# Optimization experiments

Measured on AMD Instinct MI355X. Metric: run time of the kernel, lower is better.

Reference implementation:

```python
import jax, jax.numpy as jnp
import numpy as np

B, L, D = 32, 2048, 512


def setup_inputs() -> dict:
    key = jax.random.key(0)
    kx, ka, kb, kc = jax.random.split(key, 4)
    scale = 0.5 / np.sqrt(D)  # keep recurrence spectral radius < 1 over L steps
    x = jax.random.normal(kx, (B, L, D), dtype=jnp.float32)
    deltaA = jax.random.normal(ka, (D, D), dtype=jnp.float32) * scale
    deltaB = jax.random.normal(kb, (D, D), dtype=jnp.float32) * scale
    C = jax.random.normal(kc, (D, D), dtype=jnp.float32) * scale
    return {"x": x, "deltaA": deltaA, "deltaB": deltaB, "C": C}


def reference(x, deltaA, deltaB, C):
    b, l, d = x.shape
    # Pre-project inputs with one big GEMM: u_t = x_t @ deltaB  -> [b, l, d]
    u = jnp.einsum('bld,de->ble', x, deltaB)

    def step(h, u_t):
        # h_t = h_{t-1} @ deltaA + x_t @ deltaB
        h = h @ deltaA + u_t
        return h, h

    h0 = jnp.zeros((b, d), dtype=x.dtype)
    # scan over time axis: u as [l, b, d]
    _, hs = jax.lax.scan(step, h0, jnp.swapaxes(u, 0, 1))  # hs: [l, b, d]
    # y_t = h_t @ C, one big GEMM after the scan
    y = jnp.einsum('lbd,de->lbe', hs, C)
    return jnp.swapaxes(y, 0, 1)  # [b, l, d]
```

## Files before the change

### kernel.cpp

```cpp
#include <hip/hip_runtime.h>


using bf16 = __bf16;
typedef __bf16 bf16x8 __attribute__((ext_vector_type(8)));
typedef float  f32x4  __attribute__((ext_vector_type(4)));
typedef unsigned int u32;

constexpr int Dm   = 512;
constexpr int Lseq = 2048;
constexpr int KC   = 8;
constexpr int CH   = 256;

__device__ __forceinline__ bf16x8 ld8(const bf16* p) {
  return *reinterpret_cast<const bf16x8*>(p);
}
__device__ __forceinline__ bf16x8 ld8f(const float* p) {
  f32x4 lo = *reinterpret_cast<const f32x4*>(p);
  f32x4 hi = *reinterpret_cast<const f32x4*>(p + 4);
  bf16x8 r;
#pragma unroll
  for (int i = 0; i < 4; ++i) { r[i] = (bf16)lo[i]; r[i + 4] = (bf16)hi[i]; }
  return r;
}
__device__ __forceinline__ f32x4 mfma16(bf16x8 a, bf16x8 b, f32x4 c) {
  return __builtin_amdgcn_mfma_f32_16x16x32_bf16(a, b, c, 0, 0, 0);
}
__device__ __forceinline__ void gld16(const bf16* g, bf16* l) {
  __builtin_amdgcn_global_load_lds(
      (const __attribute__((address_space(1))) u32*)g,
      (__attribute__((address_space(3))) u32*)l, 16, 0, 0);
}

template<int WM, int WN>
__device__ __forceinline__ void mma_step(const bf16* As, const bf16* Bs,
                                         int arow, int brow, int sw, int quad,
                                         f32x4 (&acc)[WM][WN]) {
#pragma unroll
  for (int ks = 0; ks < 2; ++ks) {
    const int sg = ((ks * 4 + quad) ^ sw) * 8;
    bf16x8 a[WM], b[WN];
#pragma unroll
    for (int m = 0; m < WM; ++m) a[m] = ld8(As + arow + m * 1024 + sg);
#pragma unroll
    for (int n = 0; n < WN; ++n) b[n] = ld8(Bs + brow + n * 1024 + sg);
#pragma unroll
    for (int m = 0; m < WM; ++m)
#pragma unroll
      for (int n = 0; n < WN; ++n) acc[m][n] = mfma16(a[m], b[n], acc[m][n]);
  }
}

__global__ __launch_bounds__(256) void kt_pack(
    const float* __restrict__ a, const float* __restrict__ b, const float* __restrict__ c,
    bf16* __restrict__ at, bf16* __restrict__ bt, bf16* __restrict__ ct,
    bf16* __restrict__ abf, bf16* __restrict__ zrow) {
  if (blockIdx.y == 0 && blockIdx.x == 0 && threadIdx.x < 256)
    reinterpret_cast<int*>(zrow)[threadIdx.x] = 0;
  int flat = blockIdx.x * 256 + threadIdx.x;
  int n = flat & (Dm - 1);
  int k = flat >> 9;
  const float* s = (blockIdx.y == 0) ? a : (blockIdx.y == 1) ? b : c;
  bf16* d        = (blockIdx.y == 0) ? at : (blockIdx.y == 1) ? bt : ct;
  float v = s[(long)k * Dm + n];
  d[(long)n * Dm + k] = (bf16)v;
  if (blockIdx.y == 0) abf[(long)k * Dm + n] = (bf16)v;
}

__global__ __launch_bounds__(256) void kt_cvt(
    const float* __restrict__ x, bf16* __restrict__ xb) {
  const long total = (long)32 * Lseq * Dm;
  for (long i = ((long)blockIdx.x * 256 + threadIdx.x) * 8; i < total;
       i += (long)2048 * 256 * 8)
    *reinterpret_cast<bf16x8*>(xb + i) = ld8f(x + i);
}

__global__ __launch_bounds__(256) void kt_u(
    const bf16* __restrict__ xb, const bf16* __restrict__ Bt, bf16* __restrict__ u) {
  __shared__ __align__(16) char LDSraw[36864];
  bf16* As = (bf16*)LDSraw;
  bf16* Bs = As + 128 * 64;
  const int tid = threadIdx.x, wave = tid >> 6, lane = tid & 63;
  const int quad = lane >> 4, l16 = lane & 15;
  const int seg = tid & 7, rr0 = tid >> 3;
  const int m0 = blockIdx.x * 128, n0 = blockIdx.y * 128;
  bf16* aL = As + wave * 512;
  bf16* bL = Bs + wave * 512;
  const int wrB = (wave >> 1) * 64, wcB = (wave & 1) * 64;
  const int arow = (wrB + l16) * 64, brow = (wcB + l16) * 64, sw = l16 & 7;
  f32x4 acc[4][4] = {};
  const bf16* aSrc[4]; const bf16* bSrc[4];
#pragma unroll
  for (int it = 0; it < 4; ++it) {
    int r = it * 32 + rr0;
    int sg = seg ^ (r & 7);
    aSrc[it] = xb + (long)(m0 + r) * Dm + sg * 8;
    bSrc[it] = Bt + (long)(n0 + r) * Dm + sg * 8;
  }
  for (int k0 = 0; k0 < Dm; k0 += 64) {
#pragma unroll
    for (int it = 0; it < 4; ++it) {
      gld16(aSrc[it] + k0, aL + it * 2048);
      gld16(bSrc[it] + k0, bL + it * 2048);
    }
    __syncthreads();
    mma_step<4, 4>(As, Bs, arow, brow, sw, quad, acc);
    __syncthreads();
  }
  bf16* smB = (bf16*)LDSraw;
#pragma unroll
  for (int m = 0; m < 4; ++m)
#pragma unroll
    for (int n = 0; n < 4; ++n)
#pragma unroll
      for (int r = 0; r < 4; ++r)
        smB[(wrB + m * 16 + quad * 4 + r) * 136 + wcB + n * 16 + l16] =
            (bf16)acc[m][n][r];
  __syncthreads();
#pragma unroll
  for (int it = 0; it < 8; ++it) {
    int chunk = it * 256 + tid;
    int row = chunk >> 4, c16 = chunk & 15;
    bf16x8 v = ld8(&smB[row * 136 + c16 * 8]);
    *reinterpret_cast<bf16x8*>(u + (long)(m0 + row) * Dm + n0 + c16 * 8) = v;
  }
}

__global__ __launch_bounds__(512) void kt_square(
    const bf16* __restrict__ P, const bf16* __restrict__ Pt,
    bf16* __restrict__ S, bf16* __restrict__ St) {
  const int tid = threadIdx.x;
  const int wave = tid >> 6, lane = tid & 63;
  const int quad = lane >> 4, l16 = lane & 15;
  const long rowbase = (long)blockIdx.x * 32;
  const int nbase = wave * 64;
  f32x4 acc[2][4] = {};
  for (int kk = 0; kk < Dm; kk += 32) {
    const int kf = kk + quad * 8;
    bf16x8 a0 = ld8(P + (rowbase + l16) * Dm + kf);
    bf16x8 a1 = ld8(P + (rowbase + 16 + l16) * Dm + kf);
#pragma unroll
    for (int nt = 0; nt < 4; ++nt) {
      bf16x8 bw = ld8(Pt + (long)(nbase + nt * 16 + l16) * Dm + kf);
      acc[0][nt] = mfma16(a0, bw, acc[0][nt]);
      acc[1][nt] = mfma16(a1, bw, acc[1][nt]);
    }
  }
#pragma unroll
  for (int mt = 0; mt < 2; ++mt)
#pragma unroll
    for (int nt = 0; nt < 4; ++nt)
#pragma unroll
      for (int r = 0; r < 4; ++r) {
        long m = rowbase + mt * 16 + quad * 4 + r;
        int n = nbase + nt * 16 + l16;
        float v = acc[mt][nt][r];
        S[m * Dm + n] = (bf16)v;
        St[(long)n * Dm + m] = (bf16)v;
      }
}

__global__ __launch_bounds__(512) void kt_taps(
    const bf16* __restrict__ q1, const bf16* __restrict__ q2,
    const bf16* __restrict__ q3, const bf16* __restrict__ q4,
    const bf16* __restrict__ q5, const bf16* __restrict__ q6,
    const bf16* __restrict__ q7, const bf16* __restrict__ q8,
    const bf16* __restrict__ Ct, bf16* __restrict__ Tt) {
  const int j = blockIdx.y;
  const bf16* Aop = (j == 0) ? q1 : (j == 1) ? q2 : (j == 2) ? q3 : (j == 3) ? q4
                  : (j == 4) ? q5 : (j == 5) ? q6 : (j == 6) ? q7 : q8;
  bf16* St = Tt + (long)j * Dm * Dm;
  const int tid = threadIdx.x;
  const int wave = tid >> 6, lane = tid & 63;
  const int quad = lane >> 4, l16 = lane & 15;
  const long rowbase = (long)blockIdx.x * 32;
  const int nbase = wave * 64;
  f32x4 acc[2][4] = {};
  for (int kk = 0; kk < Dm; kk += 32) {
    const int kf = kk + quad * 8;
    bf16x8 a0 = ld8(Aop + (rowbase + l16) * Dm + kf);
    bf16x8 a1 = ld8(Aop + (rowbase + 16 + l16) * Dm + kf);
#pragma unroll
    for (int nt = 0; nt < 4; ++nt) {
      bf16x8 bw = ld8(Ct + (long)(nbase + nt * 16 + l16) * Dm + kf);
      acc[0][nt] = mfma16(a0, bw, acc[0][nt]);
      acc[1][nt] = mfma16(a1, bw, acc[1][nt]);
    }
  }
#pragma unroll
  for (int mt = 0; mt < 2; ++mt)
#pragma unroll
    for (int nt = 0; nt < 4; ++nt)
#pragma unroll
      for (int r = 0; r < 4; ++r) {
        long m = rowbase + mt * 16 + quad * 4 + r;
        int n = nbase + nt * 16 + l16;
        St[(long)n * Dm + m] = (bf16)acc[mt][nt][r];
      }
}

__global__ __launch_bounds__(256) void kt_step(
    const bf16* __restrict__ u, const bf16* __restrict__ prevB,
    const bf16* __restrict__ At, bf16* __restrict__ hall, int j) {
  __shared__ __align__(16) bf16 As[64 * 64];
  __shared__ __align__(16) bf16 Bs[64 * 64];
  const int tid = threadIdx.x, wave = tid >> 6, lane = tid & 63;
  const int quad = lane >> 4, l16 = lane & 15;
  const int seg = tid & 7, rr0 = tid >> 3;
  const int m0 = blockIdx.x * 64, n0 = blockIdx.y * 64;
  const int b = m0 >> 8, c0 = m0 & 255;
  const bf16* aSrc[2]; const bf16* bSrc[2];
#pragma unroll
  for (int it = 0; it < 2; ++it) {
    int r = it * 32 + rr0;
    int sg = seg ^ (r & 7);
    aSrc[it] = prevB + ((long)b * Lseq + (long)(c0 + r) * KC + (j - 1)) * Dm + sg * 8;
    bSrc[it] = At + (long)(n0 + r) * Dm + sg * 8;
  }
  bf16* aL = As + wave * 512;
  bf16* bL = Bs + wave * 512;
  const int wrB = (wave >> 1) * 32, wcB = (wave & 1) * 32;
  const int arow = (wrB + l16) * 64, brow = (wcB + l16) * 64, sw = l16 & 7;
  f32x4 acc[2][2] = {};
  for (int k0 = 0; k0 < Dm; k0 += 64) {
#pragma unroll
    for (int it = 0; it < 2; ++it) {
      gld16(aSrc[it] + k0, aL + it * 2048);
      gld16(bSrc[it] + k0, bL + it * 2048);
    }
    __syncthreads();
    mma_step<2, 2>(As, Bs, arow, brow, sw, quad, acc);
    __syncthreads();
  }
#pragma unroll
  for (int m = 0; m < 2; ++m)
#pragma unroll
    for (int n = 0; n < 2; ++n)
#pragma unroll
      for (int r = 0; r < 4; ++r) {
        int row = wrB + m * 16 + quad * 4 + r;
        int col = n0 + wcB + n * 16 + l16;
        long off = ((long)b * Lseq + (long)(c0 + row) * KC + j) * Dm + col;
        hall[off] = (bf16)(acc[m][n][r] + (float)u[off]);
      }
}

__global__ __launch_bounds__(256) void kt_ks(
    const bf16* __restrict__ HinB, long sb, long sc, long off0,
    bf16* __restrict__ Hout, const bf16* __restrict__ Qt,
    const bf16* __restrict__ Q, const bf16* __restrict__ zrow,
    bf16* __restrict__ Snext, bf16* __restrict__ SnextT,
    int shift, int doSq) {
  __shared__ __align__(16) bf16 As[64 * 64];
  __shared__ __align__(16) bf16 Bs[64 * 64];
  const int tid = threadIdx.x, wave = tid >> 6, lane = tid & 63;
  const int quad = lane >> 4, l16 = lane & 15;
  const int seg = tid & 7, rr0 = tid >> 3;
  bf16* aL = As + wave * 512;
  bf16* bL = Bs + wave * 512;
  const int wrB = (wave >> 1) * 32, wcB = (wave & 1) * 32;
  const int arow = (wrB + l16) * 64, brow = (wcB + l16) * 64, sw = l16 & 7;
  f32x4 acc[2][2] = {};
  if (blockIdx.y < 8) {
    const int m0 = blockIdx.x * 64, n0 = blockIdx.y * 64;
    const int b = m0 >> 8, c0 = m0 & 255;
    const bf16* aSrc[2]; const bf16* bSrc[2];
#pragma unroll
    for (int it = 0; it < 2; ++it) {
      int r = it * 32 + rr0;
      int sg = seg ^ (r & 7);
      int c = c0 + r - shift;
      aSrc[it] = (c >= 0) ? HinB + ((long)b * sb + (long)c * sc + off0) * Dm + sg * 8
                          : zrow + sg * 8;
      bSrc[it] = Qt + (long)(n0 + r) * Dm + sg * 8;
    }
    for (int k0 = 0; k0 < Dm; k0 += 64) {
#pragma unroll
      for (int it = 0; it < 2; ++it) {
        gld16(aSrc[it] + k0, aL + it * 2048);
        gld16(bSrc[it] + k0, bL + it * 2048);
      }
      __syncthreads();
      mma_step<2, 2>(As, Bs, arow, brow, sw, quad, acc);
      __syncthreads();
    }
#pragma unroll
    for (int m = 0; m < 2; ++m)
#pragma unroll
      for (int n = 0; n < 2; ++n)
#pragma unroll
        for (int r = 0; r < 4; ++r) {
          int row = wrB + m * 16 + quad * 4 + r;
          int col = n0 + wcB + n * 16 + l16;
          int c = c0 + row;
          float v = acc[m][n][r] +
                    (float)HinB[((long)b * sb + (long)c * sc + off0) * Dm + col];
          Hout[((long)(b * 256 + c)) * Dm + col] = (bf16)v;
        }
  } else {
    if (blockIdx.x >= 64 || !doSq) return;
    const int m0 = (blockIdx.x >> 3) * 64, n0 = (blockIdx.x & 7) * 64;
    const bf16* aSrc[2]; const bf16* bSrc[2];
#pragma unroll
    for (int it = 0; it < 2; ++it) {
      int r = it * 32 + rr0;
      int sg = seg ^ (r & 7);
      aSrc[it] = Q + (long)(m0 + r) * Dm + sg * 8;
      bSrc[it] = Qt + (long)(n0 + r) * Dm + sg * 8;
    }
    for (int k0 = 0; k0 < Dm; k0 += 64) {
#pragma unroll
      for (int it = 0; it < 2; ++it) {
        gld16(aSrc[it] + k0, aL + it * 2048);
        gld16(bSrc[it] + k0, bL + it * 2048);
      }
      __syncthreads();
      mma_step<2, 2>(As, Bs, arow, brow, sw, quad, acc);
      __syncthreads();
    }
#pragma unroll
    for (int m = 0; m < 2; ++m)
#pragma unroll
      for (int n = 0; n < 2; ++n)
#pragma unroll
        for (int r = 0; r < 4; ++r) {
          int mg = m0 + wrB + m * 16 + quad * 4 + r;
          int ng = n0 + wcB + n * 16 + l16;
          float v = acc[m][n][r];
          Snext[(long)mg * Dm + ng] = (bf16)v;
          SnextT[(long)ng * Dm + mg] = (bf16)v;
        }
  }
}

__global__ __launch_bounds__(256) void kt_out(
    const bf16* __restrict__ hall, const bf16* __restrict__ u,
    const bf16* __restrict__ P, const bf16* __restrict__ Ct,
    const bf16* __restrict__ Tt, const bf16* __restrict__ zrow,
    float* __restrict__ y) {
  __shared__ __align__(16) char LDSraw[32768];
  bf16* As = (bf16*)LDSraw;
  bf16* Bs = As + 128 * 64;
  const int tid = threadIdx.x, wave = tid >> 6, lane = tid & 63;
  const int quad = lane >> 4, l16 = lane & 15;
  const int seg = tid & 7, rr0 = tid >> 3;
  const int m0 = blockIdx.x * 128, n0 = blockIdx.y * 128;
  const int j = blockIdx.z;
  const int b = m0 >> 8, c0 = m0 & 255;
  bf16* aL = As + wave * 512;
  bf16* bL = Bs + wave * 512;
  const int wrB = (wave >> 1) * 64, wcB = (wave & 1) * 64;
  const int arow = (wrB + l16) * 64, brow = (wcB + l16) * 64, sw = l16 & 7;
  f32x4 acc[4][4] = {};
  {
    const bf16* H0B = (j == 0) ? u : hall;
    const bf16* aSrc[4]; const bf16* bSrc[4];
#pragma unroll
    for (int it = 0; it < 4; ++it) {
      int r = it * 32 + rr0;
      int sg = seg ^ (r & 7);
      aSrc[it] = H0B + ((long)b * Lseq + (long)(c0 + r) * KC + j) * Dm + sg * 8;
      bSrc[it] = Ct + (long)(n0 + r) * Dm + sg * 8;
    }
    for (int k0 = 0; k0 < Dm; k0 += 64) {
#pragma unroll
      for (int it = 0; it < 4; ++it) {
        gld16(aSrc[it] + k0, aL + it * 2048);
        gld16(bSrc[it] + k0, bL + it * 2048);
      }
      __syncthreads();
      mma_step<4, 4>(As, Bs, arow, brow, sw, quad, acc);
      __syncthreads();
    }
  }
  {
    const bf16* Tj = Tt + (long)j * Dm * Dm;
    const bf16* aSrc[4]; const bf16* bSrc[4];
#pragma unroll
    for (int it = 0; it < 4; ++it) {
      int r = it * 32 + rr0;
      int sg = seg ^ (r & 7);
      int c = c0 + r - 1;
      aSrc[it] = (c >= 0) ? P + (long)(b * 256 + c) * Dm + sg * 8 : zrow + sg * 8;
      bSrc[it] = Tj + (long)(n0 + r) * Dm + sg * 8;
    }
    for (int k0 = 0; k0 < Dm; k0 += 64) {
#pragma unroll
      for (int it = 0; it < 4; ++it) {
        gld16(aSrc[it] + k0, aL + it * 2048);
        gld16(bSrc[it] + k0, bL + it * 2048);
      }
      __syncthreads();
      mma_step<4, 4>(As, Bs, arow, brow, sw, quad, acc);
      __syncthreads();
    }
  }
  float* sm = (float*)LDSraw;
  const int wr = wave >> 1;
#pragma unroll
  for (int p = 0; p < 2; ++p) {
    __syncthreads();
    if (wr == p) {
#pragma unroll
      for (int m = 0; m < 4; ++m)
#pragma unroll
        for (int n = 0; n < 4; ++n)
#pragma unroll
          for (int r = 0; r < 4; ++r)
            sm[(m * 16 + quad * 4 + r) * 128 + wcB + n * 16 + l16] = acc[m][n][r];
    }
    __syncthreads();
#pragma unroll
    for (int ch = 0; ch < 8; ++ch) {
      int chunk = ch * 256 + tid;
      int srow = chunk >> 5, cc = chunk & 31;
      f32x4 v = *reinterpret_cast<f32x4*>(&sm[srow * 128 + cc * 4]);
      long t = (long)(c0 + p * 64 + srow) * KC + j;
      *reinterpret_cast<f32x4*>(y + ((long)b * Lseq + t) * Dm + n0 + cc * 4) = v;
    }
  }
}

extern "C" void kernel_launch(void* const* d_in, const int* in_sizes, int n_in,
                              void* d_out, int out_size, void* d_ws, size_t ws_size,
                              hipStream_t stream) {
  const float* x  = (const float*)d_in[0];
  const float* dA = (const float*)d_in[1];
  const float* dB = (const float*)d_in[2];
  const float* Cm = (const float*)d_in[3];
  float* out = (float*)d_out;

  char* w = (char*)d_ws;
  const size_t MATB = (size_t)Dm * Dm * sizeof(bf16);
  bf16* At  = (bf16*)w; w += MATB;
  bf16* Bt  = (bf16*)w; w += MATB;
  bf16* Ct  = (bf16*)w; w += MATB;
  bf16* Abf = (bf16*)w; w += MATB;
  bf16* pw[10]; bf16* pwT[10];
  for (int l = 0; l < 10; ++l) { pw[l] = (bf16*)w; w += MATB; pwT[l] = (bf16*)w; w += MATB; }
  bf16* A3  = (bf16*)w; w += MATB;
  bf16* A3t = (bf16*)w; w += MATB;
  bf16* A5  = (bf16*)w; w += MATB;
  bf16* A6  = (bf16*)w; w += MATB;
  bf16* A7  = (bf16*)w; w += MATB;
  bf16* jkT = (bf16*)w; w += MATB;
  bf16* Tt  = (bf16*)w; w += 8 * MATB;
  bf16* zrow = (bf16*)w; w += 4096;
  bf16* u    = (bf16*)w; w += (size_t)32 * Lseq * Dm * sizeof(bf16);
  bf16* hall = (bf16*)w; w += (size_t)32 * Lseq * Dm * sizeof(bf16);
  bf16* P0 = (bf16*)w; w += (size_t)CH * 32 * Dm * sizeof(bf16);
  bf16* P1 = (bf16*)w; w += (size_t)CH * 32 * Dm * sizeof(bf16);
  bf16* xb = hall;

  kt_pack<<<dim3(Dm * Dm / 256, 3), 256, 0, stream>>>(dA, dB, Cm, At, Bt, Ct, Abf, zrow);
  kt_cvt<<<2048, 256, 0, stream>>>(x, xb);
  kt_u<<<dim3(512, 4), 256, 0, stream>>>(xb, Bt, u);
  kt_square<<<Dm / 32, 512, 0, stream>>>(Abf, At, pw[0], pwT[0]);
  kt_square<<<Dm / 32, 512, 0, stream>>>(pw[0], pwT[0], pw[1], pwT[1]);
  kt_square<<<Dm / 32, 512, 0, stream>>>(pw[1], pwT[1], pw[2], pwT[2]);
  kt_square<<<Dm / 32, 512, 0, stream>>>(pw[0], At,     A3, A3t);
  kt_square<<<Dm / 32, 512, 0, stream>>>(pw[1], At,     A5, jkT);
  kt_square<<<Dm / 32, 512, 0, stream>>>(pw[1], pwT[0], A6, jkT);
  kt_square<<<Dm / 32, 512, 0, stream>>>(pw[1], A3t,    A7, jkT);
  kt_taps<<<dim3(Dm / 32, 8), 512, 0, stream>>>(Abf, pw[0], A3, pw[1], A5, A6, A7, pw[2], Ct, Tt);
  for (int j = 1; j < KC; ++j)
    kt_step<<<dim3(128, 8), 256, 0, stream>>>(u, (j == 1) ? u : hall, At, hall, j);
  kt_ks<<<dim3(128, 9), 256, 0, stream>>>(hall, (long)Lseq, (long)KC, (long)(KC - 1),
                                          P0, pwT[2], pw[2], zrow, pw[3], pwT[3], 1, 1);
  bf16* hin = P0; bf16* hout = P1;
  for (int i = 1; i < 8; ++i) {
    int nx = (3 + i < 10) ? 3 + i : 9;
    kt_ks<<<dim3(128, 9), 256, 0, stream>>>(hin, 256L, 1L, 0L, hout, pwT[2 + i], pw[2 + i],
                                            zrow, pw[nx], pwT[nx], 1 << i, (i < 7) ? 1 : 0);
    bf16* tmp = hin; hin = hout; hout = tmp;
  }
  kt_out<<<dim3(64, 4, 8), 256, 0, stream>>>(hall, u, hin, Ct, Tt, zrow, out);
}
```

Measured before the change: 733.3 us.

## Replace serial intra-chunk step kernels with log-depth tree and batch matrix squarings

The seven sequential per-step kernels inside each 8-step chunk become three launches that compute several steps at once. Each later step is built from an earlier state plus precomputed powers A, A^2, A^3, A^4 applied to u, using larger 128x128 tiles and an LDS-staged epilogue. Independent matrix-power GEMMs are also grouped into batched launches via a job struct. This cuts launch count and serial dependency depth, in exchange for more total GEMM work in later tree levels and more bf16 rounding through the extra power products.

```diff
diff --git a/kernel.cpp b/kernel.cpp
--- a/kernel.cpp
+++ b/kernel.cpp
@@ -125,9 +125,10 @@
   }
 }
 
-__global__ __launch_bounds__(512) void kt_square(
-    const bf16* __restrict__ P, const bf16* __restrict__ Pt,
-    bf16* __restrict__ S, bf16* __restrict__ St) {
+struct SqJob { const bf16* P; const bf16* Pt; bf16* S; bf16* St; };
+struct SqJobs { SqJob j[4]; };
+__global__ __launch_bounds__(512) void kt_sqz(SqJobs jobs) {
+  const SqJob jb = jobs.j[blockIdx.y];
   const int tid = threadIdx.x;
   const int wave = tid >> 6, lane = tid & 63;
   const int quad = lane >> 4, l16 = lane & 15;
@@ -136,11 +137,11 @@
   f32x4 acc[2][4] = {};
   for (int kk = 0; kk < Dm; kk += 32) {
     const int kf = kk + quad * 8;
-    bf16x8 a0 = ld8(P + (rowbase + l16) * Dm + kf);
-    bf16x8 a1 = ld8(P + (rowbase + 16 + l16) * Dm + kf);
+    bf16x8 a0 = ld8(jb.P + (rowbase + l16) * Dm + kf);
+    bf16x8 a1 = ld8(jb.P + (rowbase + 16 + l16) * Dm + kf);
 #pragma unroll
     for (int nt = 0; nt < 4; ++nt) {
-      bf16x8 bw = ld8(Pt + (long)(nbase + nt * 16 + l16) * Dm + kf);
+      bf16x8 bw = ld8(jb.Pt + (long)(nbase + nt * 16 + l16) * Dm + kf);
       acc[0][nt] = mfma16(a0, bw, acc[0][nt]);
       acc[1][nt] = mfma16(a1, bw, acc[1][nt]);
     }
@@ -154,8 +155,8 @@
         long m = rowbase + mt * 16 + quad * 4 + r;
         int n = nbase + nt * 16 + l16;
         float v = acc[mt][nt][r];
-        S[m * Dm + n] = (bf16)v;
-        St[(long)n * Dm + m] = (bf16)v;
+        jb.S[m * Dm + n] = (bf16)v;
+        jb.St[(long)n * Dm + m] = (bf16)v;
       }
 }
 
@@ -198,50 +199,83 @@
       }
 }
 
-__global__ __launch_bounds__(256) void kt_step(
-    const bf16* __restrict__ u, const bf16* __restrict__ prevB,
-    const bf16* __restrict__ At, bf16* __restrict__ hall, int j) {
-  __shared__ __align__(16) bf16 As[64 * 64];
-  __shared__ __align__(16) bf16 Bs[64 * 64];
+__global__ __launch_bounds__(256) void kt_tree(
+    const bf16* __restrict__ u, const bf16* __restrict__ hall,
+    const bf16* __restrict__ At, const bf16* __restrict__ A2t,
+    const bf16* __restrict__ A3t, const bf16* __restrict__ A4t,
+    bf16* __restrict__ out, int base, int j0) {
+  __shared__ __align__(16) char LDSraw[32768];
+  bf16* As = (bf16*)LDSraw;
+  bf16* Bs = As + 128 * 64;
   const int tid = threadIdx.x, wave = tid >> 6, lane = tid & 63;
   const int quad = lane >> 4, l16 = lane & 15;
   const int seg = tid & 7, rr0 = tid >> 3;
-  const int m0 = blockIdx.x * 64, n0 = blockIdx.y * 64;
+  const int m0 = blockIdx.x * 128, n0 = blockIdx.y * 128;
+  const int j = j0 + (int)blockIdx.z;
   const int b = m0 >> 8, c0 = m0 & 255;
-  const bf16* aSrc[2]; const bf16* bSrc[2];
-#pragma unroll
-  for (int it = 0; it < 2; ++it) {
-    int r = it * 32 + rr0;
-    int sg = seg ^ (r & 7);
-    aSrc[it] = prevB + ((long)b * Lseq + (long)(c0 + r) * KC + (j - 1)) * Dm + sg * 8;
-    bSrc[it] = At + (long)(n0 + r) * Dm + sg * 8;
-  }
   bf16* aL = As + wave * 512;
   bf16* bL = Bs + wave * 512;
-  const int wrB = (wave >> 1) * 32, wcB = (wave & 1) * 32;
+  const int wrB = (wave >> 1) * 64, wcB = (wave & 1) * 64;
   const int arow = (wrB + l16) * 64, brow = (wcB + l16) * 64, sw = l16 & 7;
-  f32x4 acc[2][2] = {};
-  for (int k0 = 0; k0 < Dm; k0 += 64) {
-#pragma unroll
-    for (int it = 0; it < 2; ++it) {
-      gld16(aSrc[it] + k0, aL + it * 2048);
-      gld16(bSrc[it] + k0, bL + it * 2048);
-    }
+  f32x4 acc[4][4] = {};
+  const int nseg = j - base;
+  for (int s = 0; s < nseg; ++s) {
+    const int p = j - base - s;
+    const bf16* tp = (p == 1) ? At : (p == 2) ? A2t : (p == 3) ? A3t : A4t;
+    const int tsel = (s == 0) ? base : base + s;
+    const bf16* srcB = (s == 0 && base > 0) ? hall : u;
+    const bf16* aSrc[4]; const bf16* bSrc[4];
+#pragma unroll
+    for (int it = 0; it < 4; ++it) {
+      int r = it * 32 + rr0;
+      int sg = seg ^ (r & 7);
+      aSrc[it] = srcB + ((long)b * Lseq + (long)(c0 + r) * KC + tsel) * Dm + sg * 8;
+      bSrc[it] = tp + (long)(n0 + r) * Dm + sg * 8;
+    }
+    for (int k0 = 0; k0 < Dm; k0 += 64) {
+#pragma unroll
+      for (int it = 0; it < 4; ++it) {
+        gld16(aSrc[it] + k0, aL + it * 2048);
+        gld16(bSrc[it] + k0, bL + it * 2048);
+      }
+      __syncthreads();
+      mma_step<4, 4>(As, Bs, arow, brow, sw, quad, acc);
+      __syncthreads();
+    }
+  }
+  float* sm = (float*)LDSraw;
+  const int wr = wave >> 1;
+#pragma unroll
+  for (int ppass = 0; ppass < 2; ++ppass) {
     __syncthreads();
-    mma_step<2, 2>(As, Bs, arow, brow, sw, quad, acc);
+    if (wr == ppass) {
+#pragma unroll
+      for (int m = 0; m < 4; ++m)
+#pragma unroll
+        for (int n = 0; n < 4; ++n)
+#pragma unroll
+          for (int r = 0; r < 4; ++r)
+            sm[(m * 16 + quad * 4 + r) * 128 + wcB + n * 16 + l16] = acc[m][n][r];
+    }
     __syncthreads();
-  }
-#pragma unroll
-  for (int m = 0; m < 2; ++m)
-#pragma unroll
-    for (int n = 0; n < 2; ++n)
-#pragma unroll
-      for (int r = 0; r < 4; ++r) {
-        int row = wrB + m * 16 + quad * 4 + r;
-        int col = n0 + wcB + n * 16 + l16;
-        long off = ((long)b * Lseq + (long)(c0 + row) * KC + j) * Dm + col;
-        hall[off] = (bf16)(acc[m][n][r] + (float)u[off]);
-      }
+#pragma unroll
+    for (int it = 0; it < 4; ++it) {
+      int chunk = it * 256 + tid;
+      int row = chunk >> 4, cg = chunk & 15;
+      f32x4 lo = *reinterpret_cast<f32x4*>(&sm[row * 128 + cg * 8]);
+      f32x4 hi = *reinterpret_cast<f32x4*>(&sm[row * 128 + cg * 8 + 4]);
+      long gaddr = ((long)b * Lseq + (long)(c0 + ppass * 64 + row) * KC + j) * Dm
+                   + n0 + cg * 8;
+      bf16x8 uv = ld8(u + gaddr);
+      bf16x8 o;
+#pragma unroll
+      for (int i = 0; i < 4; ++i) {
+        o[i]     = (bf16)(lo[i] + (float)uv[i]);
+        o[i + 4] = (bf16)(hi[i] + (float)uv[i + 4]);
+      }
+      *reinterpret_cast<bf16x8*>(out + gaddr) = o;
+    }
+  }
 }
 
 __global__ __launch_bounds__(256) void kt_ks(
@@ -454,16 +488,23 @@
   kt_pack<<<dim3(Dm * Dm / 256, 3), 256, 0, stream>>>(dA, dB, Cm, At, Bt, Ct, Abf, zrow);
   kt_cvt<<<2048, 256, 0, stream>>>(x, xb);
   kt_u<<<dim3(512, 4), 256, 0, stream>>>(xb, Bt, u);
-  kt_square<<<Dm / 32, 512, 0, stream>>>(Abf, At, pw[0], pwT[0]);
-  kt_square<<<Dm / 32, 512, 0, stream>>>(pw[0], pwT[0], pw[1], pwT[1]);
-  kt_square<<<Dm / 32, 512, 0, stream>>>(pw[1], pwT[1], pw[2], pwT[2]);
-  kt_square<<<Dm / 32, 512, 0, stream>>>(pw[0], At,     A3, A3t);
-  kt_square<<<Dm / 32, 512, 0, stream>>>(pw[1], At,     A5, jkT);
-  kt_square<<<Dm / 32, 512, 0, stream>>>(pw[1], pwT[0], A6, jkT);
-  kt_square<<<Dm / 32, 512, 0, stream>>>(pw[1], A3t,    A7, jkT);
+  {
+    SqJobs s1 = {{{Abf, At, pw[0], pwT[0]}, {}, {}, {}}};
+    kt_sqz<<<dim3(Dm / 32, 1), 512, 0, stream>>>(s1);
+    SqJobs s2 = {{{pw[0], At, A3, A3t},
+                  {pw[0], pwT[0], pw[1], pwT[1]},
+                  {}, {}}};
+    kt_sqz<<<dim3(Dm / 32, 2), 512, 0, stream>>>(s2);
+    SqJobs s3 = {{{pw[1], At, A5, jkT},
+                  {pw[1], pwT[0], A6, jkT},
+                  {pw[1], A3t, A7, jkT},
+                  {pw[1], pwT[1], pw[2], pwT[2]}}};
+    kt_sqz<<<dim3(Dm / 32, 4), 512, 0, stream>>>(s3);
+  }
   kt_taps<<<dim3(Dm / 32, 8), 512, 0, stream>>>(Abf, pw[0], A3, pw[1], A5, A6, A7, pw[2], Ct, Tt);
-  for (int j = 1; j < KC; ++j)
-    kt_step<<<dim3(128, 8), 256, 0, stream>>>(u, (j == 1) ? u : hall, At, hall, j);
+  kt_tree<<<dim3(64, 4, 1), 256, 0, stream>>>(u, hall, At, pwT[0], A3t, pwT[1], hall, 0, 1);
+  kt_tree<<<dim3(64, 4, 2), 256, 0, stream>>>(u, hall, At, pwT[0], A3t, pwT[1], hall, 1, 2);
+  kt_tree<<<dim3(64, 4, 4), 256, 0, stream>>>(u, hall, At, pwT[0], A3t, pwT[1], hall, 3, 4);
   kt_ks<<<dim3(128, 9), 256, 0, stream>>>(hall, (long)Lseq, (long)KC, (long)(KC - 1),
                                           P0, pwT[2], pw[2], zrow, pw[3], pwT[3], 1, 1);
   bf16* hin = P0; bf16* hout = P1;
```

Measured after the change: 674.6 us. 8.0% less time.
